# Kernel optimization log

Hardware: AMD Instinct MI355X
Metric: run time of the kernel (lower is better)

Reference implementation:

```python
import jax, jax.numpy as jnp
import numpy as np
from jax import lax

B, C, W = 16, 64, 125000  # batch, EEG channels, raw samples
KH, KW, SW, OC = 3, 2500, 1250, 32


def setup_inputs() -> dict:
    key = jax.random.key(0)
    ks = jax.random.split(key, 10)
    inp = {
        "x": jax.random.normal(ks[0], (B, 1, C, W), dtype=jnp.float32),
        # Conv2d(1->32, kernel=(3,2500))
        "conv_w": jax.random.normal(ks[1], (OC, 1, KH, KW), dtype=jnp.float32) * 0.02,
        "conv_b": jax.random.normal(ks[2], (OC,), dtype=jnp.float32) * 0.02,
        # Conv2d(32->1, kernel=(1,1))
        "conv2_w": jax.random.normal(ks[3], (1, OC, 1, 1), dtype=jnp.float32) * 0.1,
        "conv2_b": jax.random.normal(ks[4], (1,), dtype=jnp.float32) * 0.1,
        # nn.RNN(input_size=1, hidden_size=1): scalar weights
        "w_ih": jax.random.normal(ks[5], (1, 1), dtype=jnp.float32),
        "w_hh": jax.random.normal(ks[6], (1, 1), dtype=jnp.float32),
        "b_ih": jax.random.normal(ks[7], (1,), dtype=jnp.float32) * 0.1,
        "b_hh": jax.random.normal(ks[8], (1,), dtype=jnp.float32) * 0.1,
        # torch.rand(num_layers=1, B, 1) hidden init, reused for every row i
        "h0": jax.random.uniform(ks[9], (1, B, 1), dtype=jnp.float32),
    }
    return inp


def reference(x, conv_w, conv_b, conv2_w, conv2_b, w_ih, w_hh, b_ih, b_hh, h0):
    # F.pad(x, (0,0,1,1), 'replicate'): pad channel (height) dim by 1 each side
    xp = jnp.pad(x, ((0, 0), (0, 0), (1, 1), (0, 0)), mode="edge")
    # conv + relu -> [B, 32, C, T]
    y = lax.conv_general_dilated(
        xp, conv_w, window_strides=(1, SW), padding="VALID",
        dimension_numbers=("NCHW", "OIHW", "NCHW"))
    y = jax.nn.relu(y + conv_b[None, :, None, None])
    # 1x1 conv 32->1 + relu -> [B, C, T]
    z = jnp.einsum("bohw,o->bhw", y, conv2_w[0, :, 0, 0]) + conv2_b[0]
    z = jax.nn.relu(z)
    # Elman RNN with scalar weights, scanned over T; carry is [B, C]
    wih, whh = w_ih[0, 0], w_hh[0, 0]
    bias = b_ih[0] + b_hh[0]
    h_init = jnp.broadcast_to(h0[0, :, 0][:, None], z.shape[:2])  # [B, C]

    def step(h, xt):  # xt: [B, C]
        h = jnp.tanh(wih * xt + whh * h + bias)
        return h, None

    xs = jnp.moveaxis(z, -1, 0)  # [T, B, C]
    h_final, _ = lax.scan(step, h_init, xs)
    return jax.nn.sigmoid(h_final)  # [B, C]
```

## Files before the change

### kernel.cpp

```cpp
#include <hip/hip_runtime.h>
#include <math.h>

#define B_ 16
#define C_ 64
#define J_ 100
#define T_ 99
#define KW_ 1250
#define N_ 192
#define M_ (B_*C_*J_)
#define BM 128
#define BK 32
#define NCHUNK 40

typedef __attribute__((ext_vector_type(8))) _Float16 half8;
typedef __attribute__((ext_vector_type(4))) _Float16 half4_t;
typedef __attribute__((ext_vector_type(4))) float f32x4;
typedef __attribute__((ext_vector_type(4), aligned(4))) float f32x4u;

template <typename PT>
__global__ __launch_bounds__(256) void gemm_kernel(const float* __restrict__ x,
                                                   const float* __restrict__ cw,
                                                   PT* __restrict__ P)
{
    __shared__ __align__(16) _Float16 Abf[BM][BK + 8];
    __shared__ __align__(16) _Float16 Bbf[N_][BK + 8];

    const int tid  = threadIdx.x;
    const int bm0  = blockIdx.x * BM;
    const int lane = tid & 63;
    const int wave = tid >> 6;
    const int wm   = (wave & 1) * 64;
    const int wn   = (wave >> 1) * 96;
    const int l15  = lane & 15;
    const int lq   = lane >> 4;

    const float* aptr[4]; int adst[4]; int aqc[4];
#pragma unroll
    for (int i = 0; i < 4; i++) {
        int q = i * 256 + tid;
        int r = q >> 3, qc = q & 7;
        aptr[i] = x + (size_t)(bm0 + r) * KW_ + qc * 4;
        adst[i] = r * (BK + 8) + qc * 4;
        aqc[i]  = qc * 4;
    }
    const float* bptr[6]; int bdst[6]; int bqc[6];
#pragma unroll
    for (int i = 0; i < 6; i++) {
        int q = i * 256 + tid;
        int n = q >> 3, qc = q & 7;
        int o = n / 6, rem = n - o * 6, kh = rem >> 1, hf = rem & 1;
        bptr[i] = cw + o * 7500 + kh * 2500 + hf * 1250 + qc * 4;
        bdst[i] = n * (BK + 8) + qc * 4;
        bqc[i]  = qc * 4;
    }

    f32x4 acc[4][6];
#pragma unroll
    for (int mi = 0; mi < 4; mi++)
#pragma unroll
        for (int ni = 0; ni < 6; ni++) acc[mi][ni] = (f32x4){0.f, 0.f, 0.f, 0.f};

    _Float16* As = &Abf[0][0];
    _Float16* Bs = &Bbf[0][0];

    for (int ck = 0; ck < NCHUNK; ck++) {
        const int k0 = ck * BK;
#pragma unroll
        for (int i = 0; i < 4; i++) {
            float vv[4];
            if (k0 + aqc[i] + 3 < KW_) {
                f32x4u t4 = *(const f32x4u*)(aptr[i] + k0);
                vv[0] = t4.x; vv[1] = t4.y; vv[2] = t4.z; vv[3] = t4.w;
            } else {
#pragma unroll
                for (int u = 0; u < 4; u++) {
                    int k = k0 + aqc[i] + u;
                    vv[u] = (k < KW_) ? aptr[i][k0 + u] : 0.f;
                }
            }
            half4_t s4;
            s4.x = (_Float16)vv[0]; s4.y = (_Float16)vv[1];
            s4.z = (_Float16)vv[2]; s4.w = (_Float16)vv[3];
            *(half4_t*)(As + adst[i]) = s4;
        }
#pragma unroll
        for (int i = 0; i < 6; i++) {
            float vv[4];
            if (k0 + bqc[i] + 3 < KW_) {
                f32x4u t4 = *(const f32x4u*)(bptr[i] + k0);
                vv[0] = t4.x; vv[1] = t4.y; vv[2] = t4.z; vv[3] = t4.w;
            } else {
#pragma unroll
                for (int u = 0; u < 4; u++) {
                    int k = k0 + bqc[i] + u;
                    vv[u] = (k < KW_) ? bptr[i][k0 + u] : 0.f;
                }
            }
            half4_t s4;
            s4.x = (_Float16)vv[0]; s4.y = (_Float16)vv[1];
            s4.z = (_Float16)vv[2]; s4.w = (_Float16)vv[3];
            *(half4_t*)(Bs + bdst[i]) = s4;
        }
        __syncthreads();

        half8 afr[4], bfr[6];
#pragma unroll
        for (int mi = 0; mi < 4; mi++)
            afr[mi] = *(const half8*)&Abf[wm + mi * 16 + l15][lq * 8];
#pragma unroll
        for (int ni = 0; ni < 6; ni++)
            bfr[ni] = *(const half8*)&Bbf[wn + ni * 16 + l15][lq * 8];
#pragma unroll
        for (int mi = 0; mi < 4; mi++)
#pragma unroll
            for (int ni = 0; ni < 6; ni++)
                acc[mi][ni] = __builtin_amdgcn_mfma_f32_16x16x32_f16(
                    afr[mi], bfr[ni], acc[mi][ni], 0, 0, 0);
        __syncthreads();
    }

#pragma unroll
    for (int mi = 0; mi < 4; mi++) {
        int mrow = bm0 + wm + mi * 16 + lq * 4;
#pragma unroll
        for (int ni = 0; ni < 6; ni++) {
            int n = wn + ni * 16 + l15;
#pragma unroll
            for (int r2 = 0; r2 < 4; r2++)
                P[(size_t)(mrow + r2) * N_ + n] = (PT)acc[mi][ni][r2];
        }
    }
}

template <typename PT>
__global__ __launch_bounds__(256) void combine_kernel(const PT* __restrict__ P,
                                                      const float* __restrict__ conv_b,
                                                      const float* __restrict__ c2w,
                                                      const float* __restrict__ c2b,
                                                      float* __restrict__ z)
{
    __shared__ float Pl[64][196];
    __shared__ float red[4][64];
    const int t   = blockIdx.x;
    const int b   = blockIdx.y;
    const int tid = threadIdx.x;
    const int c   = tid & 63;
    const int og  = tid >> 6;

    float v[8];
#pragma unroll
    for (int o = 0; o < 8; o++) v[o] = conv_b[og * 8 + o];

    for (int hf = 0; hf < 2; hf++) {
        const int j = t + hf;
        __syncthreads();
        for (int idx = tid; idx < 64 * N_; idx += 256) {
            int r = idx / N_, nn = idx - r * N_;
            Pl[r][nn] = (float)P[((size_t)((b * 64 + r) * J_ + j)) * N_ + nn];
        }
        __syncthreads();
#pragma unroll
        for (int kh = 0; kh < 3; kh++) {
            int r = c + kh - 1;
            r = r < 0 ? 0 : (r > 63 ? 63 : r);
#pragma unroll
            for (int o = 0; o < 8; o++)
                v[o] += Pl[r][(og * 8 + o) * 6 + kh * 2 + hf];
        }
    }

    float part = 0.f;
#pragma unroll
    for (int o = 0; o < 8; o++) part += fmaxf(v[o], 0.f) * c2w[og * 8 + o];
    red[og][c] = part;
    __syncthreads();
    if (og == 0) {
        float zz = red[0][c] + red[1][c] + red[2][c] + red[3][c] + c2b[0];
        z[(size_t)(b * 64 + c) * T_ + t] = fmaxf(zz, 0.f);
    }
}

__global__ __launch_bounds__(256) void rnn_kernel(const float* __restrict__ z,
                                                  const float* __restrict__ w_ih,
                                                  const float* __restrict__ w_hh,
                                                  const float* __restrict__ b_ih,
                                                  const float* __restrict__ b_hh,
                                                  const float* __restrict__ h0,
                                                  float* __restrict__ out)
{
    int g = blockIdx.x * 256 + threadIdx.x;
    if (g >= B_ * C_) return;
    int b = g >> 6;
    const float wih  = w_ih[0];
    const float whh  = w_hh[0];
    const float bias = b_ih[0] + b_hh[0];
    float h = h0[b];
    const float* zp = z + (size_t)g * T_;
    for (int t = 0; t < T_; t++)
        h = tanhf(fmaf(wih, zp[t], fmaf(whh, h, bias)));
    out[g] = 1.f / (1.f + expf(-h));
}

extern "C" void kernel_launch(void* const* d_in, const int* in_sizes, int n_in,
                              void* d_out, int out_size, void* d_ws, size_t ws_size,
                              hipStream_t stream)
{
    const float* x   = (const float*)d_in[0];
    const float* cw  = (const float*)d_in[1];
    const float* cb  = (const float*)d_in[2];
    const float* c2w = (const float*)d_in[3];
    const float* c2b = (const float*)d_in[4];
    const float* wih = (const float*)d_in[5];
    const float* whh = (const float*)d_in[6];
    const float* bih = (const float*)d_in[7];
    const float* bhh = (const float*)d_in[8];
    const float* h0  = (const float*)d_in[9];
    float* out = (float*)d_out;

    const size_t pbytes_f32 = (size_t)M_ * N_ * sizeof(float);
    const size_t pbytes_f16 = (size_t)M_ * N_ * sizeof(_Float16);
    const size_t zbytes     = (size_t)B_ * C_ * T_ * sizeof(float);

    if (ws_size >= pbytes_f32 + zbytes) {
        float* P = (float*)d_ws;
        float* z = (float*)((char*)d_ws + pbytes_f32);
        gemm_kernel<float><<<M_ / BM, 256, 0, stream>>>(x, cw, P);
        combine_kernel<float><<<dim3(T_, B_), 256, 0, stream>>>(P, cb, c2w, c2b, z);
        rnn_kernel<<<4, 256, 0, stream>>>(z, wih, whh, bih, bhh, h0, out);
    } else if (ws_size >= pbytes_f16 + zbytes) {
        _Float16* P = (_Float16*)d_ws;
        float* z = (float*)((char*)d_ws + pbytes_f16);
        gemm_kernel<_Float16><<<M_ / BM, 256, 0, stream>>>(x, cw, P);
        combine_kernel<_Float16><<<dim3(T_, B_), 256, 0, stream>>>(P, cb, c2w, c2b, z);
        rnn_kernel<<<4, 256, 0, stream>>>(z, wih, whh, bih, bhh, h0, out);
    }
}
```

Measured before the change: 861.0 us.

## Pre-convert weights to fp16 and double-buffer GEMM with direct global-to-LDS loads

A new kernel converts the conv weights once per call into a zero-padded fp16 buffer. The GEMM then streams B tiles straight into LDS with global_load_lds and prefetches A two chunks ahead in registers, using double-buffered shared memory so one barrier per chunk suffices. This targets the repeated per-block fp32-to-fp16 conversion of weights and the load/compute serialization, at the cost of an extra launch, a larger workspace requirement and an unpadded LDS layout that may cause bank conflicts. The fp16 P fallback path is removed, so the code returns early if the workspace is too small.

```diff
diff --git a/kernel.cpp b/kernel.cpp
--- a/kernel.cpp
+++ b/kernel.cpp
@@ -6,6 +6,7 @@
 #define J_ 100
 #define T_ 99
 #define KW_ 1250
+#define KP_ 1280
 #define N_ 192
 #define M_ (B_*C_*J_)
 #define BM 128
@@ -13,17 +14,28 @@
 #define NCHUNK 40
 
 typedef __attribute__((ext_vector_type(8))) _Float16 half8;
-typedef __attribute__((ext_vector_type(4))) _Float16 half4_t;
 typedef __attribute__((ext_vector_type(4))) float f32x4;
-typedef __attribute__((ext_vector_type(4), aligned(4))) float f32x4u;
-
-template <typename PT>
-__global__ __launch_bounds__(256) void gemm_kernel(const float* __restrict__ x,
-                                                   const float* __restrict__ cw,
-                                                   PT* __restrict__ P)
-{
-    __shared__ __align__(16) _Float16 Abf[BM][BK + 8];
-    __shared__ __align__(16) _Float16 Bbf[N_][BK + 8];
+typedef __attribute__((ext_vector_type(2), aligned(8))) float f32x2;
+
+#define GLD_LDS16(gp, lp) \
+    __builtin_amdgcn_global_load_lds((const __attribute__((address_space(1))) void*)(gp), \
+                                     (__attribute__((address_space(3))) void*)(lp), 16, 0, 0)
+
+__global__ __launch_bounds__(256) void wconv_kernel(const float* __restrict__ cw,
+                                                    _Float16* __restrict__ wh)
+{
+    int n = blockIdx.x;
+    int o = n / 6, rem = n - o * 6, kh = rem >> 1, hf = rem & 1;
+    const float* src = cw + o * 7500 + kh * 2500 + hf * 1250;
+    for (int k = threadIdx.x; k < KP_; k += 256)
+        wh[n * KP_ + k] = (k < KW_) ? (_Float16)src[k] : (_Float16)0.f;
+}
+
+__global__ __launch_bounds__(256, 2) void gemm_kernel(const float* __restrict__ x,
+                                                      const _Float16* __restrict__ wh,
+                                                      float* __restrict__ P)
+{
+    __shared__ __align__(16) _Float16 sm[2][(BM + N_) * BK];
 
     const int tid  = threadIdx.x;
     const int bm0  = blockIdx.x * BM;
@@ -34,24 +46,22 @@
     const int l15  = lane & 15;
     const int lq   = lane >> 4;
 
-    const float* aptr[4]; int adst[4]; int aqc[4];
-#pragma unroll
-    for (int i = 0; i < 4; i++) {
-        int q = i * 256 + tid;
-        int r = q >> 3, qc = q & 7;
-        aptr[i] = x + (size_t)(bm0 + r) * KW_ + qc * 4;
-        adst[i] = r * (BK + 8) + qc * 4;
-        aqc[i]  = qc * 4;
-    }
-    const float* bptr[6]; int bdst[6]; int bqc[6];
-#pragma unroll
-    for (int i = 0; i < 6; i++) {
-        int q = i * 256 + tid;
-        int n = q >> 3, qc = q & 7;
-        int o = n / 6, rem = n - o * 6, kh = rem >> 1, hf = rem & 1;
-        bptr[i] = cw + o * 7500 + kh * 2500 + hf * 1250 + qc * 4;
-        bdst[i] = n * (BK + 8) + qc * 4;
-        bqc[i]  = qc * 4;
+    const float* ap[2]; int koff[2]; int adst[2];
+#pragma unroll
+    for (int u = 0; u < 2; u++) {
+        int q = u * 256 + tid;
+        int r = q >> 2, p = q & 3;
+        ap[u]   = x + (size_t)(bm0 + r) * KW_ + p * 8;
+        koff[u] = p * 8;
+        adst[u] = q * 8;
+    }
+    const _Float16* bp[3]; int bdst[3];
+#pragma unroll
+    for (int i = 0; i < 3; i++) {
+        int qb = (i * 4 + wave) * 64 + lane;
+        int n = qb >> 2, p = qb & 3;
+        bp[i]   = wh + n * KP_ + p * 8;
+        bdst[i] = (i * 4 + wave) * 512;
     }
 
     f32x4 acc[4][6];
@@ -60,63 +70,65 @@
 #pragma unroll
         for (int ni = 0; ni < 6; ni++) acc[mi][ni] = (f32x4){0.f, 0.f, 0.f, 0.f};
 
-    _Float16* As = &Abf[0][0];
-    _Float16* Bs = &Bbf[0][0];
+    f32x2 areg[2][2][4];
+#define LOADA(k0, slot)                                                        \
+    do {                                                                       \
+        _Pragma("unroll") for (int u = 0; u < 2; u++)                          \
+        _Pragma("unroll") for (int j = 0; j < 4; j++) {                        \
+            int k = (k0) + koff[u] + j * 2;            \
+            areg[slot][u][j] = (k + 2 <= KW_)                                  \
+                ? *(const f32x2*)(ap[u] + (k0) + j * 2)                        \
+                : (f32x2){0.f, 0.f};                                           \
+        }                                                                      \
+    } while (0)
+
+    LOADA(0, 0);
+    LOADA(BK, 1);
+    {
+        _Float16* Bb = &sm[0][BM * BK];
+#pragma unroll
+        for (int i = 0; i < 3; i++) GLD_LDS16(bp[i], Bb + bdst[i]);
+    }
 
     for (int ck = 0; ck < NCHUNK; ck++) {
-        const int k0 = ck * BK;
-#pragma unroll
-        for (int i = 0; i < 4; i++) {
-            float vv[4];
-            if (k0 + aqc[i] + 3 < KW_) {
-                f32x4u t4 = *(const f32x4u*)(aptr[i] + k0);
-                vv[0] = t4.x; vv[1] = t4.y; vv[2] = t4.z; vv[3] = t4.w;
-            } else {
-#pragma unroll
-                for (int u = 0; u < 4; u++) {
-                    int k = k0 + aqc[i] + u;
-                    vv[u] = (k < KW_) ? aptr[i][k0 + u] : 0.f;
-                }
+        const int slot = ck & 1;
+        _Float16* Ab = &sm[slot][0];
+        _Float16* Bb = &sm[slot][BM * BK];
+
+#pragma unroll
+        for (int u = 0; u < 2; u++) {
+            half8 h;
+#pragma unroll
+            for (int j = 0; j < 4; j++) {
+                h[2 * j]     = (_Float16)areg[slot][u][j].x;
+                h[2 * j + 1] = (_Float16)areg[slot][u][j].y;
             }
-            half4_t s4;
-            s4.x = (_Float16)vv[0]; s4.y = (_Float16)vv[1];
-            s4.z = (_Float16)vv[2]; s4.w = (_Float16)vv[3];
-            *(half4_t*)(As + adst[i]) = s4;
-        }
-#pragma unroll
-        for (int i = 0; i < 6; i++) {
-            float vv[4];
-            if (k0 + bqc[i] + 3 < KW_) {
-                f32x4u t4 = *(const f32x4u*)(bptr[i] + k0);
-                vv[0] = t4.x; vv[1] = t4.y; vv[2] = t4.z; vv[3] = t4.w;
-            } else {
-#pragma unroll
-                for (int u = 0; u < 4; u++) {
-                    int k = k0 + bqc[i] + u;
-                    vv[u] = (k < KW_) ? bptr[i][k0 + u] : 0.f;
-                }
-            }
-            half4_t s4;
-            s4.x = (_Float16)vv[0]; s4.y = (_Float16)vv[1];
-            s4.z = (_Float16)vv[2]; s4.w = (_Float16)vv[3];
-            *(half4_t*)(Bs + bdst[i]) = s4;
-        }
+            *(half8*)(Ab + adst[u]) = h;
+        }
+
         __syncthreads();
 
+        if (ck + 2 < NCHUNK) LOADA((ck + 2) * BK, slot);
+        if (ck + 1 < NCHUNK) {
+            _Float16* Bn = &sm[slot ^ 1][BM * BK];
+            const int k1 = (ck + 1) * BK;
+#pragma unroll
+            for (int i = 0; i < 3; i++) GLD_LDS16(bp[i] + k1, Bn + bdst[i]);
+        }
+
         half8 afr[4], bfr[6];
 #pragma unroll
         for (int mi = 0; mi < 4; mi++)
-            afr[mi] = *(const half8*)&Abf[wm + mi * 16 + l15][lq * 8];
+            afr[mi] = *(const half8*)(Ab + (wm + mi * 16 + l15) * BK + lq * 8);
 #pragma unroll
         for (int ni = 0; ni < 6; ni++)
-            bfr[ni] = *(const half8*)&Bbf[wn + ni * 16 + l15][lq * 8];
+            bfr[ni] = *(const half8*)(Bb + (wn + ni * 16 + l15) * BK + lq * 8);
 #pragma unroll
         for (int mi = 0; mi < 4; mi++)
 #pragma unroll
             for (int ni = 0; ni < 6; ni++)
                 acc[mi][ni] = __builtin_amdgcn_mfma_f32_16x16x32_f16(
                     afr[mi], bfr[ni], acc[mi][ni], 0, 0, 0);
-        __syncthreads();
     }
 
 #pragma unroll
@@ -127,13 +139,13 @@
             int n = wn + ni * 16 + l15;
 #pragma unroll
             for (int r2 = 0; r2 < 4; r2++)
-                P[(size_t)(mrow + r2) * N_ + n] = (PT)acc[mi][ni][r2];
-        }
-    }
-}
-
-template <typename PT>
-__global__ __launch_bounds__(256) void combine_kernel(const PT* __restrict__ P,
+                P[(size_t)(mrow + r2) * N_ + n] = acc[mi][ni][r2];
+        }
+    }
+#undef LOADA
+}
+
+__global__ __launch_bounds__(256) void combine_kernel(const float* __restrict__ P,
                                                       const float* __restrict__ conv_b,
                                                       const float* __restrict__ c2w,
                                                       const float* __restrict__ c2b,
@@ -156,7 +168,7 @@
         __syncthreads();
         for (int idx = tid; idx < 64 * N_; idx += 256) {
             int r = idx / N_, nn = idx - r * N_;
-            Pl[r][nn] = (float)P[((size_t)((b * 64 + r) * J_ + j)) * N_ + nn];
+            Pl[r][nn] = P[((size_t)((b * 64 + r) * J_ + j)) * N_ + nn];
         }
         __syncthreads();
 #pragma unroll
@@ -217,21 +229,18 @@
     const float* h0  = (const float*)d_in[9];
     float* out = (float*)d_out;
 
-    const size_t pbytes_f32 = (size_t)M_ * N_ * sizeof(float);
-    const size_t pbytes_f16 = (size_t)M_ * N_ * sizeof(_Float16);
-    const size_t zbytes     = (size_t)B_ * C_ * T_ * sizeof(float);
-
-    if (ws_size >= pbytes_f32 + zbytes) {
-        float* P = (float*)d_ws;
-        float* z = (float*)((char*)d_ws + pbytes_f32);
-        gemm_kernel<float><<<M_ / BM, 256, 0, stream>>>(x, cw, P);
-        combine_kernel<float><<<dim3(T_, B_), 256, 0, stream>>>(P, cb, c2w, c2b, z);
-        rnn_kernel<<<4, 256, 0, stream>>>(z, wih, whh, bih, bhh, h0, out);
-    } else if (ws_size >= pbytes_f16 + zbytes) {
-        _Float16* P = (_Float16*)d_ws;
-        float* z = (float*)((char*)d_ws + pbytes_f16);
-        gemm_kernel<_Float16><<<M_ / BM, 256, 0, stream>>>(x, cw, P);
-        combine_kernel<_Float16><<<dim3(T_, B_), 256, 0, stream>>>(P, cb, c2w, c2b, z);
-        rnn_kernel<<<4, 256, 0, stream>>>(z, wih, whh, bih, bhh, h0, out);
-    }
-}
+    const size_t whbytes = (size_t)N_ * KP_ * sizeof(_Float16);
+    const size_t pbytes  = (size_t)M_ * N_ * sizeof(float);
+    const size_t zbytes  = (size_t)B_ * C_ * T_ * sizeof(float);
+
+    if (ws_size < whbytes + pbytes + zbytes) return;
+
+    _Float16* wh = (_Float16*)d_ws;
+    float* P = (float*)((char*)d_ws + whbytes);
+    float* z = (float*)((char*)d_ws + whbytes + pbytes);
+
+    wconv_kernel<<<N_, 256, 0, stream>>>(cw, wh);
+    gemm_kernel<<<M_ / BM, 256, 0, stream>>>(x, wh, P);
+    combine_kernel<<<dim3(T_, B_), 256, 0, stream>>>(P, cb, c2w, c2b, z);
+    rnn_kernel<<<4, 256, 0, stream>>>(z, wih, whh, bih, bhh, h0, out);
+}
```

After: 840.4 us. -2.4%, faster.
